# Kernel optimization log

Measured on AMD Instinct MI355X. Metric: run time of the kernel, lower is better.

Reference implementation:

```python
import jax, jax.numpy as jnp
import numpy as np

B, L, H, DEPTH, IN_DIM = 1024, 32, 128, 2, 2
LOG_PROB_FACTOR = 0.5


def setup_inputs() -> dict:
    key = jax.random.key(0)
    ks = jax.random.split(key, 7)
    s = 0.1  # ~variance_scaling(0.1) magnitude
    return {
        "x": jax.random.randint(ks[0], (B, L, L), 0, IN_DIM, dtype=jnp.int32),
        "WH": jax.random.normal(ks[1], (DEPTH, H, H), jnp.float32) * s,   # horizontal-carry Dense per layer
        "WV": jax.random.normal(ks[2], (DEPTH, H, H), jnp.float32) * s,   # vertical-carry Dense per layer
        "WS0": jax.random.normal(ks[3], (2 * IN_DIM, H), jnp.float32) * s,  # state Dense, layer 0 (input concat)
        "WS1": jax.random.normal(ks[4], (H, H), jnp.float32) * s,          # state Dense, layer 1
        "Wout": jax.random.normal(ks[5], (H, IN_DIM - 1), jnp.float32) * s,  # outputDense kernel
        "bout": jnp.zeros((IN_DIM - 1,), jnp.float32),                        # outputDense bias
    }


def _forward(x, WH, WV, WS0, WS1, Wout, bout):
    elu = jax.nn.elu

    def log_probs(logCoeffs):  # (IN_DIM-1,) -> (IN_DIM,) ; realValuedOutput=True so no phase
        amp = jnp.concatenate([jnp.zeros((1,), logCoeffs.dtype), logCoeffs])
        return LOG_PROB_FACTOR * jax.nn.log_softmax(amp)

    direction = jnp.asarray(np.where(np.arange(L) % 2 == 0, 1, -1).astype(np.int32))  # boustrophedon scan

    def single(xs):  # xs: (L, L) int lattice
        onehot = jax.nn.one_hot(xs, IN_DIM, dtype=jnp.float32)  # (L, L, IN_DIM)

        def row_step(carry, row_in):
            carryStates, prevLine = carry  # (L, DEPTH, H), (L, IN_DIM)
            line_oh, b = row_in            # (L, IN_DIM), scalar direction
            rev = lambda z: jnp.where(b == 1, z, jnp.flip(z, 0))
            carryV_all = rev(carryStates)                 # vertical carries from previous row
            line_r = rev(line_oh)
            xH_all = jnp.concatenate([jnp.zeros((1, IN_DIM), line_r.dtype), line_r], 0)[:-1]  # shifted inputs
            xV_all = rev(prevLine)                         # previous row one-hots

            def site_step(carryH, site_in):  # carryH: (DEPTH, H)
                carryV, xH, xV = site_in     # (DEPTH,H), (IN_DIM,), (IN_DIM,)
                state = jnp.concatenate([xH, xV])  # (2*IN_DIM,)
                h0 = elu(carryH[0] @ WH[0] + carryV[0] @ WV[0] + state @ WS0)
                h1 = elu(carryH[1] @ WH[1] + carryV[1] @ WV[1] + h0 @ WS1)
                newCarry = jnp.stack([h0, h1])  # (DEPTH, H)
                logCoeff = log_probs(h1 @ Wout + bout)  # (IN_DIM,)
                return newCarry, (newCarry, logCoeff)

            _, (carries, logCoeffs) = jax.lax.scan(
                site_step, jnp.zeros((DEPTH, H), jnp.float32), (carryV_all, xH_all, xV_all))
            logProb = jnp.sum(rev(logCoeffs) * line_oh, axis=-1)  # (L,)
            return (rev(carries), line_oh), jnp.nan_to_num(logProb, nan=-35.0)

        _, probs = jax.lax.scan(
            row_step,
            (jnp.zeros((L, DEPTH, H), jnp.float32), jnp.zeros((L, IN_DIM), jnp.float32)),
            (onehot, direction))
        return jnp.sum(probs)  # scalar log-amplitude per sample

    return jax.vmap(single)(x)  # (B,)


def reference(x, WH, WV, WS0, WS1, Wout, bout):
    return _forward(x, WH, WV, WS0, WS1, Wout, bout)
```

## Files before the change

### kernel.cpp

```cpp
#include <hip/hip_runtime.h>
#include <math.h>

#define LL  32
#define HH  128
#define NQ  4
#define NS  4
#define KPT 32

__global__ __launch_bounds__(512, 2)
void rnn2d_kernel(const int* __restrict__ x,
                  const float* __restrict__ WH,
                  const float* __restrict__ WV,
                  const float* __restrict__ WS0,
                  const float* __restrict__ WS1,
                  const float* __restrict__ Wout,
                  const float* __restrict__ bout,
                  float* __restrict__ out)
{
    __shared__ float carry[NS][LL][2][HH];
    __shared__ float Pa[NS][NQ][HH];
    __shared__ float Pb[NS][NQ][HH];
    __shared__ float zbuf[2][HH];
    __shared__ float red[NS][2];
    __shared__ int   xrow[NS][LL];
    __shared__ int   xprev[NS][LL];

    const int tid = threadIdx.x;
    const int j   = tid & (HH - 1);
    const int q   = tid >> 7;
    const int k0  = q * KPT;
    const int b4  = blockIdx.x * NS;

    float wh0[KPT], wv0[KPT], wh1[KPT], wv1[KPT], ws1r[KPT];
#pragma unroll
    for (int i = 0; i < KPT; ++i) {
        const int k = k0 + i;
        wh0[i]  = WH[k * HH + j];
        wv0[i]  = WV[k * HH + j];
        wh1[i]  = WH[(HH + k) * HH + j];
        wv1[i]  = WV[(HH + k) * HH + j];
        ws1r[i] = WS1[k * HH + j];
    }
#pragma unroll
    for (int i = 0; i < KPT; ++i)
        asm volatile("" : "+v"(wh0[i]), "+v"(wv0[i]), "+v"(wh1[i]),
                          "+v"(wv1[i]), "+v"(ws1r[i]));

    const float s0a = WS0[0 * HH + j];
    const float s0b = WS0[1 * HH + j];
    const float s0c = WS0[2 * HH + j];
    const float s0d = WS0[3 * HH + j];
    const float wo  = Wout[j];
    const float bo  = bout[0];

    for (int i = tid; i < NS * LL * 2 * HH; i += 512) ((float*)carry)[i] = 0.0f;
    if (tid < 2 * HH) ((float*)zbuf)[tid] = 0.0f;

    float total = 0.0f;

#pragma unroll 1
    for (int r = 0; r < LL; ++r) {
        if (tid < NS * LL) {
            xrow[tid >> 5][tid & 31] = x[(b4 + (tid >> 5)) * (LL * LL) + r * LL + (tid & 31)];
        } else if (tid < 2 * NS * LL) {
            const int t2 = tid - NS * LL;
            xprev[t2 >> 5][t2 & 31] =
                (r > 0) ? x[(b4 + (t2 >> 5)) * (LL * LL) + (r - 1) * LL + (t2 & 31)] : 0;
        }
        __syncthreads();

        const int dir = (r & 1) ? -1 : 1;
#pragma unroll 1
        for (int p = 0; p < LL; ++p) {
            const int c  = (dir == 1) ? p : (LL - 1 - p);
            const int cp = c - dir;

#pragma unroll
            for (int smp = 0; smp < NS; ++smp) {
                const float* cH = (p == 0) ? &zbuf[0][0] : &carry[smp][cp][0][0];
                const float* cV = &carry[smp][c][0][0];
                float a0 = 0.f, a1 = 0.f, a2 = 0.f, a3 = 0.f;
                float e0 = 0.f, e1 = 0.f, e2 = 0.f, e3 = 0.f;
#pragma unroll
                for (int i = 0; i < KPT; i += 4) {
                    const float4 h0 = *(const float4*)(cH + k0 + i);
                    const float4 v0 = *(const float4*)(cV + k0 + i);
                    const float4 h1 = *(const float4*)(cH + HH + k0 + i);
                    const float4 v1 = *(const float4*)(cV + HH + k0 + i);
                    a0 = fmaf(h0.x, wh0[i + 0], a0);
                    a1 = fmaf(h0.y, wh0[i + 1], a1);
                    a2 = fmaf(h0.z, wh0[i + 2], a2);
                    a3 = fmaf(h0.w, wh0[i + 3], a3);
                    a0 = fmaf(v0.x, wv0[i + 0], a0);
                    a1 = fmaf(v0.y, wv0[i + 1], a1);
                    a2 = fmaf(v0.z, wv0[i + 2], a2);
                    a3 = fmaf(v0.w, wv0[i + 3], a3);
                    e0 = fmaf(h1.x, wh1[i + 0], e0);
                    e1 = fmaf(h1.y, wh1[i + 1], e1);
                    e2 = fmaf(h1.z, wh1[i + 2], e2);
                    e3 = fmaf(h1.w, wh1[i + 3], e3);
                    e0 = fmaf(v1.x, wv1[i + 0], e0);
                    e1 = fmaf(v1.y, wv1[i + 1], e1);
                    e2 = fmaf(v1.z, wv1[i + 2], e2);
                    e3 = fmaf(v1.w, wv1[i + 3], e3);
                }
                Pa[smp][q][j] = (a0 + a1) + (a2 + a3);
                Pb[smp][q][j] = (e0 + e1) + (e2 + e3);
            }
            __syncthreads();

            {
                float s = (Pa[q][0][j] + Pa[q][1][j]) + (Pa[q][2][j] + Pa[q][3][j]);
                if (p > 0) s += (xrow[q][cp] == 0) ? s0a : s0b;
                if (r > 0) s += (xprev[q][c] == 0) ? s0c : s0d;
                s = (s > 0.f) ? s : expm1f(s);
                carry[q][c][0][j] = s;
            }
            __syncthreads();

#pragma unroll
            for (int smp = 0; smp < NS; ++smp) {
                const float* h0p = &carry[smp][c][0][0];
                float a0 = 0.f, a1 = 0.f, a2 = 0.f, a3 = 0.f;
#pragma unroll
                for (int i = 0; i < KPT; i += 4) {
                    const float4 s4 = *(const float4*)(h0p + k0 + i);
                    a0 = fmaf(s4.x, ws1r[i + 0], a0);
                    a1 = fmaf(s4.y, ws1r[i + 1], a1);
                    a2 = fmaf(s4.z, ws1r[i + 2], a2);
                    a3 = fmaf(s4.w, ws1r[i + 3], a3);
                }
                Pa[smp][q][j] = (a0 + a1) + (a2 + a3);
            }
            __syncthreads();

            int xc = 0;
            {
                float t = (Pa[q][0][j] + Pa[q][1][j]) + (Pa[q][2][j] + Pa[q][3][j])
                        + (Pb[q][0][j] + Pb[q][1][j]) + (Pb[q][2][j] + Pb[q][3][j]);
                t = (t > 0.f) ? t : expm1f(t);
                carry[q][c][1][j] = t;
                float g = t * wo;
#pragma unroll
                for (int off = 32; off > 0; off >>= 1)
                    g += __shfl_down(g, off, 64);
                if ((j & 63) == 0) red[q][j >> 6] = g;
                xc = xrow[q][c];
            }
            __syncthreads();

            if (j == 0) {
                const float t  = red[q][0] + red[q][1] + bo;
                const float sp = fmaxf(t, 0.f) + log1pf(expf(-fabsf(t)));
                total += 0.5f * (((xc == 1) ? t : 0.f) - sp);
            }
        }
    }
    if (j == 0) out[b4 + q] = total;
}

extern "C" void kernel_launch(void* const* d_in, const int* in_sizes, int n_in,
                              void* d_out, int out_size, void* d_ws, size_t ws_size,
                              hipStream_t stream) {
    rnn2d_kernel<<<dim3(1024 / NS), dim3(512), 0, stream>>>(
        (const int*)  d_in[0],
        (const float*)d_in[1],
        (const float*)d_in[2],
        (const float*)d_in[3],
        (const float*)d_in[4],
        (const float*)d_in[5],
        (const float*)d_in[6],
        (float*)d_out);
}
```

Measured before the change: 4.504 ms.

## Split K across eight thread groups and move layer-1 carry products into second phase

Doubles the block to 1024 threads so each thread handles 16 rows of K instead of 32, halving per-thread register weight storage. The layer-1 horizontal and vertical carry products now run in the second phase together with the WS1 product, which balances the two phases and removes the separate Pb buffer and the zero buffer. This trades more threads per block and a wider 8-way reduction in LDS for shorter per-thread FMA chains and higher occupancy. Only half the threads do the reduction and ELU steps.

New measurement: 10.56 ms. 2.34x slower.

```diff
diff --git a/kernel.cpp b/kernel.cpp
--- a/kernel.cpp
+++ b/kernel.cpp
@@ -3,11 +3,11 @@
 
 #define LL  32
 #define HH  128
-#define NQ  4
+#define NQ  8
 #define NS  4
-#define KPT 32
+#define KPT 16
 
-__global__ __launch_bounds__(512, 2)
+__global__ __launch_bounds__(1024, 4)
 void rnn2d_kernel(const int* __restrict__ x,
                   const float* __restrict__ WH,
                   const float* __restrict__ WV,
@@ -18,9 +18,7 @@
                   float* __restrict__ out)
 {
     __shared__ float carry[NS][LL][2][HH];
-    __shared__ float Pa[NS][NQ][HH];
-    __shared__ float Pb[NS][NQ][HH];
-    __shared__ float zbuf[2][HH];
+    __shared__ float P[NS][NQ][HH];
     __shared__ float red[NS][2];
     __shared__ int   xrow[NS][LL];
     __shared__ int   xprev[NS][LL];
@@ -46,15 +44,15 @@
         asm volatile("" : "+v"(wh0[i]), "+v"(wv0[i]), "+v"(wh1[i]),
                           "+v"(wv1[i]), "+v"(ws1r[i]));
 
-    const float s0a = WS0[0 * HH + j];
-    const float s0b = WS0[1 * HH + j];
-    const float s0c = WS0[2 * HH + j];
-    const float s0d = WS0[3 * HH + j];
-    const float wo  = Wout[j];
-    const float bo  = bout[0];
+    float s0a = WS0[0 * HH + j];
+    float s0b = WS0[1 * HH + j];
+    float s0c = WS0[2 * HH + j];
+    float s0d = WS0[3 * HH + j];
+    float wo  = Wout[j];
+    float bo  = bout[0];
+    asm volatile("" : "+v"(s0a), "+v"(s0b), "+v"(s0c), "+v"(s0d), "+v"(wo), "+v"(bo));
 
-    for (int i = tid; i < NS * LL * 2 * HH; i += 512) ((float*)carry)[i] = 0.0f;
-    if (tid < 2 * HH) ((float*)zbuf)[tid] = 0.0f;
+    for (int i = tid; i < NS * LL * 2 * HH; i += 1024) ((float*)carry)[i] = 0.0f;
 
     float total = 0.0f;
 
@@ -72,45 +70,37 @@
         const int dir = (r & 1) ? -1 : 1;
 #pragma unroll 1
         for (int p = 0; p < LL; ++p) {
-            const int c  = (dir == 1) ? p : (LL - 1 - p);
-            const int cp = c - dir;
+            const int c   = (dir == 1) ? p : (LL - 1 - p);
+            const int cp  = c - dir;
+            const int cps = (p == 0) ? c : cp;
 
 #pragma unroll
             for (int smp = 0; smp < NS; ++smp) {
-                const float* cH = (p == 0) ? &zbuf[0][0] : &carry[smp][cp][0][0];
+                const float* cH = &carry[smp][cps][0][0];
                 const float* cV = &carry[smp][c][0][0];
                 float a0 = 0.f, a1 = 0.f, a2 = 0.f, a3 = 0.f;
-                float e0 = 0.f, e1 = 0.f, e2 = 0.f, e3 = 0.f;
 #pragma unroll
                 for (int i = 0; i < KPT; i += 4) {
-                    const float4 h0 = *(const float4*)(cH + k0 + i);
-                    const float4 v0 = *(const float4*)(cV + k0 + i);
-                    const float4 h1 = *(const float4*)(cH + HH + k0 + i);
-                    const float4 v1 = *(const float4*)(cV + HH + k0 + i);
-                    a0 = fmaf(h0.x, wh0[i + 0], a0);
-                    a1 = fmaf(h0.y, wh0[i + 1], a1);
-                    a2 = fmaf(h0.z, wh0[i + 2], a2);
-                    a3 = fmaf(h0.w, wh0[i + 3], a3);
-                    a0 = fmaf(v0.x, wv0[i + 0], a0);
-                    a1 = fmaf(v0.y, wv0[i + 1], a1);
-                    a2 = fmaf(v0.z, wv0[i + 2], a2);
-                    a3 = fmaf(v0.w, wv0[i + 3], a3);
-                    e0 = fmaf(h1.x, wh1[i + 0], e0);
-                    e1 = fmaf(h1.y, wh1[i + 1], e1);
-                    e2 = fmaf(h1.z, wh1[i + 2], e2);
-                    e3 = fmaf(h1.w, wh1[i + 3], e3);
-                    e0 = fmaf(v1.x, wv1[i + 0], e0);
-                    e1 = fmaf(v1.y, wv1[i + 1], e1);
-                    e2 = fmaf(v1.z, wv1[i + 2], e2);
-                    e3 = fmaf(v1.w, wv1[i + 3], e3);
+                    const float4 v4 = *(const float4*)(cV + k0 + i);
+                    float4 h4;
+                    if (p > 0) h4 = *(const float4*)(cH + k0 + i);
+                    else       h4 = make_float4(0.f, 0.f, 0.f, 0.f);
+                    a0 = fmaf(h4.x, wh0[i + 0], a0);
+                    a1 = fmaf(h4.y, wh0[i + 1], a1);
+                    a2 = fmaf(h4.z, wh0[i + 2], a2);
+                    a3 = fmaf(h4.w, wh0[i + 3], a3);
+                    a0 = fmaf(v4.x, wv0[i + 0], a0);
+                    a1 = fmaf(v4.y, wv0[i + 1], a1);
+                    a2 = fmaf(v4.z, wv0[i + 2], a2);
+                    a3 = fmaf(v4.w, wv0[i + 3], a3);
                 }
-                Pa[smp][q][j] = (a0 + a1) + (a2 + a3);
-                Pb[smp][q][j] = (e0 + e1) + (e2 + e3);
+                P[smp][q][j] = (a0 + a1) + (a2 + a3);
             }
             __syncthreads();
 
-            {
-                float s = (Pa[q][0][j] + Pa[q][1][j]) + (Pa[q][2][j] + Pa[q][3][j]);
+            if (q < 4) {
+                float s = ((P[q][0][j] + P[q][1][j]) + (P[q][2][j] + P[q][3][j]))
+                        + ((P[q][4][j] + P[q][5][j]) + (P[q][6][j] + P[q][7][j]));
                 if (p > 0) s += (xrow[q][cp] == 0) ? s0a : s0b;
                 if (r > 0) s += (xprev[q][c] == 0) ? s0c : s0d;
                 s = (s > 0.f) ? s : expm1f(s);
@@ -120,49 +110,63 @@
 
 #pragma unroll
             for (int smp = 0; smp < NS; ++smp) {
+                const float* cH1 = &carry[smp][cps][1][0];
+                const float* cV1 = &carry[smp][c][1][0];
                 const float* h0p = &carry[smp][c][0][0];
                 float a0 = 0.f, a1 = 0.f, a2 = 0.f, a3 = 0.f;
 #pragma unroll
                 for (int i = 0; i < KPT; i += 4) {
+                    const float4 v4 = *(const float4*)(cV1 + k0 + i);
                     const float4 s4 = *(const float4*)(h0p + k0 + i);
+                    float4 h4;
+                    if (p > 0) h4 = *(const float4*)(cH1 + k0 + i);
+                    else       h4 = make_float4(0.f, 0.f, 0.f, 0.f);
+                    a0 = fmaf(h4.x, wh1[i + 0], a0);
+                    a1 = fmaf(h4.y, wh1[i + 1], a1);
+                    a2 = fmaf(h4.z, wh1[i + 2], a2);
+                    a3 = fmaf(h4.w, wh1[i + 3], a3);
+                    a0 = fmaf(v4.x, wv1[i + 0], a0);
+                    a1 = fmaf(v4.y, wv1[i + 1], a1);
+                    a2 = fmaf(v4.z, wv1[i + 2], a2);
+                    a3 = fmaf(v4.w, wv1[i + 3], a3);
                     a0 = fmaf(s4.x, ws1r[i + 0], a0);
                     a1 = fmaf(s4.y, ws1r[i + 1], a1);
                     a2 = fmaf(s4.z, ws1r[i + 2], a2);
                     a3 = fmaf(s4.w, ws1r[i + 3], a3);
                 }
-                Pa[smp][q][j] = (a0 + a1) + (a2 + a3);
+                P[smp][q][j] = (a0 + a1) + (a2 + a3);
             }
             __syncthreads();
 
             int xc = 0;
-            {
-                float t = (Pa[q][0][j] + Pa[q][1][j]) + (Pa[q][2][j] + Pa[q][3][j])
-                        + (Pb[q][0][j] + Pb[q][1][j]) + (Pb[q][2][j] + Pb[q][3][j]);
+            if (q < 4) {
+                float t = ((P[q][0][j] + P[q][1][j]) + (P[q][2][j] + P[q][3][j]))
+                        + ((P[q][4][j] + P[q][5][j]) + (P[q][6][j] + P[q][7][j]));
                 t = (t > 0.f) ? t : expm1f(t);
                 carry[q][c][1][j] = t;
                 float g = t * wo;
 #pragma unroll
                 for (int off = 32; off > 0; off >>= 1)
                     g += __shfl_down(g, off, 64);
-                if ((j & 63) == 0) red[q][j >> 6] = g;
+                if ((tid & 63) == 0) red[q][(tid >> 6) & 1] = g;
                 xc = xrow[q][c];
             }
             __syncthreads();
 
-            if (j == 0) {
+            if (q < 4 && j == 0) {
                 const float t  = red[q][0] + red[q][1] + bo;
                 const float sp = fmaxf(t, 0.f) + log1pf(expf(-fabsf(t)));
                 total += 0.5f * (((xc == 1) ? t : 0.f) - sp);
             }
         }
     }
-    if (j == 0) out[b4 + q] = total;
+    if (q < 4 && j == 0) out[b4 + q] = total;
 }
 
 extern "C" void kernel_launch(void* const* d_in, const int* in_sizes, int n_in,
                               void* d_out, int out_size, void* d_ws, size_t ws_size,
                               hipStream_t stream) {
-    rnn2d_kernel<<<dim3(1024 / NS), dim3(512), 0, stream>>>(
+    rnn2d_kernel<<<dim3(1024 / NS), dim3(1024), 0, stream>>>(
         (const int*)  d_in[0],
         (const float*)d_in[1],
         (const float*)d_in[2],
```
